# Performance work log

Hardware: AMD Instinct MI355X
Metric: run time of the kernel (lower is better)

## Reference

```python
import jax, jax.numpy as jnp
import numpy as np

EMBED = 128   # embed_dim
HEADS = 8
POINTS = 4
H_SP, W_SP = 51, 102   # hardcoded spatial_shapes in __init__
BEV = 100              # bev_res
HRES = 50              # height_res


def _make_ref_points():
    """Exact numpy replica of the spherical grid built in __init__."""
    eps = 1e-6
    x = np.linspace(-71 / 2, 71 / 2, BEV)
    y = np.linspace(-71 / 2, 71 / 2, BEV)
    z = np.linspace(-50 / 2, 50 / 2, HRES)
    gx, gy, gz = np.meshgrid(x, y, z, indexing='ij')
    phi = np.sign(gy + eps) * np.arccos(gx / (np.sqrt(gx ** 2 + gy ** 2) + eps))
    theta = np.arccos(gz / (np.sqrt(gx ** 2 + gy ** 2 + gz ** 2) + eps))
    phi = 2 * np.pi - phi
    phi[phi > 2 * np.pi] -= 2 * np.pi
    col = phi / (2 * np.pi)   # grd_col_cross
    row = theta / np.pi       # grd_row_cross
    ref = np.stack([col, row], axis=-1)              # (BEV, BEV, HRES, 2)
    ref = ref.transpose(2, 0, 1, 3).reshape(HRES, BEV * BEV, 2)
    return jnp.asarray(ref, dtype=jnp.float32)


def setup_inputs() -> dict:
    key = jax.random.key(0)
    ks = jax.random.split(key, 12)
    d = EMBED
    s = 0.02
    return {
        'query': jax.random.normal(ks[0], (1, BEV * BEV, d), jnp.float32),
        'value': jax.random.normal(ks[1], (1, H_SP * W_SP, d), jnp.float32),
        'ref_points': _make_ref_points(),
        'W_off': jax.random.normal(ks[2], (d, HEADS * POINTS * 2), jnp.float32) * s,
        'b_off': jax.random.normal(ks[3], (HEADS * POINTS * 2,), jnp.float32) * s,
        'W_attn': jax.random.normal(ks[4], (d, HEADS * POINTS), jnp.float32) * s,
        'b_attn': jax.random.normal(ks[5], (HEADS * POINTS,), jnp.float32) * s,
        'W_val': jax.random.normal(ks[6], (d, d), jnp.float32) * s,
        'b_val': jax.random.normal(ks[7], (d,), jnp.float32) * s,
        'W_out': jax.random.normal(ks[8], (d, d), jnp.float32) * s,
        'b_out': jax.random.normal(ks[9], (d,), jnp.float32) * s,
        'W_proj': jax.random.normal(ks[10], (d, 1), jnp.float32) * s,
        'b_proj': jax.random.normal(ks[11], (1,), jnp.float32) * s,
    }


def _bilinear_sample(vflat, loc):
    """grid_sample(bilinear, zero padding, align_corners=False).
    vflat: (B, H*W, hd) value maps; loc: (B, N, 2) normalized [0,1] (x,y)."""
    px = loc[..., 0] * W_SP - 0.5
    py = loc[..., 1] * H_SP - 0.5
    x0 = jnp.floor(px)
    y0 = jnp.floor(py)
    dx = (px - x0)[..., None]
    dy = (py - y0)[..., None]
    x0i = x0.astype(jnp.int32)
    y0i = y0.astype(jnp.int32)

    def gather(xi, yi):
        valid = (xi >= 0) & (xi < W_SP) & (yi >= 0) & (yi < H_SP)
        idx = jnp.clip(yi, 0, H_SP - 1) * W_SP + jnp.clip(xi, 0, W_SP - 1)
        v = jnp.take_along_axis(vflat, idx[..., None], axis=1)  # (B, N, hd)
        return v * valid[..., None].astype(vflat.dtype)

    v00 = gather(x0i, y0i)
    v01 = gather(x0i + 1, y0i)
    v10 = gather(x0i, y0i + 1)
    v11 = gather(x0i + 1, y0i + 1)
    return (v00 * (1 - dx) * (1 - dy) + v01 * dx * (1 - dy)
            + v10 * (1 - dx) * dy + v11 * dx * dy)


def reference(query, value, ref_points, W_off, b_off, W_attn, b_attn,
              W_val, b_val, W_out, b_out, W_proj, b_proj):
    bs, nq, d = query.shape
    hd = d // HEADS
    L = ref_points.shape[0]

    # query-dependent MSDA projections (identical across height levels)
    offsets = (query @ W_off + b_off).reshape(bs, nq, HEADS, POINTS, 2)
    aw = jax.nn.softmax((query @ W_attn + b_attn).reshape(bs, nq, HEADS, POINTS), axis=-1)
    awt = aw.transpose(0, 2, 1, 3)                              # (bs, heads, nq, points)
    v = (value @ W_val + b_val).reshape(bs, -1, HEADS, hd)
    vflat = v.transpose(0, 2, 1, 3).reshape(bs * HEADS, H_SP * W_SP, hd)
    norm = jnp.asarray([W_SP, H_SP], dtype=query.dtype)         # offset_normalizer [W, H]

    def per_level(ref):  # ref: (nq, 2) -> MSDA output with its internal residual
        loc = ref[None, :, None, None, :] + offsets / norm      # (bs, nq, heads, pts, 2)
        loc = loc.transpose(0, 2, 1, 3, 4).reshape(bs * HEADS, nq * POINTS, 2)
        samp = _bilinear_sample(vflat, loc).reshape(bs, HEADS, nq, POINTS, hd)
        out = jnp.einsum('bhnp,bhnpd->bnhd', awt, samp).reshape(bs, nq, d)
        return out @ W_out + b_out + query                      # mmcv MSDA adds identity

    grd = jax.vmap(per_level)(ref_points)                       # (L, bs, nq, d)
    grd_3d = grd.transpose(1, 2, 0, 3).reshape(bs, BEV, BEV, L, d)
    weights = jax.nn.softmax(grd_3d @ W_proj + b_proj, axis=3)  # (bs, BEV, BEV, L, 1)
    max_height_index = jnp.argmax(weights, axis=3)              # (bs, BEV, BEV, 1)
    grd_bev = (weights * grd_3d).sum(axis=3)                    # (bs, BEV, BEV, d)
    return grd_bev.reshape(bs, nq, d) + query, max_height_index
```

## Files before the change

### kernel.cpp

```cpp
#include <hip/hip_runtime.h>
#include <hip/hip_fp16.h>
#include <math.h>

#define EMBED   128
#define NHEADS  8
#define NPOINTS 4
#define HD      16
#define HSP     51
#define WSP     102
#define NPIX    (HSP * WSP)
#define NQ      10000
#define NLVL    50

struct h4v { __half2 a; __half2 b; };

__device__ __forceinline__ float4 h4_to_f4(h4v v) {
    const float2 lo = __half22float2(v.a);
    const float2 hi = __half22float2(v.b);
    float4 r; r.x = lo.x; r.y = lo.y; r.z = hi.x; r.w = hi.y;
    return r;
}

#define GRID_A ((NPIX + 7) / 8)
#define GRID_B (NQ / 8)

__global__ __launch_bounds__(256) void k_prep(
    const float* __restrict__ value,
    const float* __restrict__ Wv,
    const float* __restrict__ bv,
    const float* __restrict__ query,
    const float* __restrict__ Woff,
    const float* __restrict__ boff,
    const float* __restrict__ Wattn,
    const float* __restrict__ battn,
    const float* __restrict__ Wout,
    const float* __restrict__ Wproj,
    __half* __restrict__ vout,
    float* __restrict__ gout,
    float* __restrict__ off_out,
    float* __restrict__ aw_out) {
    const int b = blockIdx.x;
    const int t = threadIdx.x;
    __shared__ float srow[8][EMBED];
    __shared__ float4 u_s[32];

    if (b < GRID_A) {
        const int p   = t >> 5;
        const int s   = t & 31;
        const int pix = b * 8 + p;
        const int pl  = min(pix, NPIX - 1);
        *(float4*)&srow[p][s * 4] =
            *(const float4*)(value + (size_t)pl * EMBED + s * 4);
        if (t < 32) {
            float4 u4 = {0.f, 0.f, 0.f, 0.f};
            const float* w0 = Wout + (size_t)(t * 4 + 0) * EMBED;
            const float* w1 = Wout + (size_t)(t * 4 + 1) * EMBED;
            const float* w2 = Wout + (size_t)(t * 4 + 2) * EMBED;
            const float* w3 = Wout + (size_t)(t * 4 + 3) * EMBED;
#pragma unroll 4
            for (int d = 0; d < EMBED; d += 4) {
                const float4 wp = *(const float4*)(Wproj + d);
                const float4 a = *(const float4*)(w0 + d);
                const float4 c = *(const float4*)(w1 + d);
                const float4 e = *(const float4*)(w2 + d);
                const float4 f = *(const float4*)(w3 + d);
                u4.x = fmaf(a.x, wp.x, u4.x); u4.x = fmaf(a.y, wp.y, u4.x);
                u4.x = fmaf(a.z, wp.z, u4.x); u4.x = fmaf(a.w, wp.w, u4.x);
                u4.y = fmaf(c.x, wp.x, u4.y); u4.y = fmaf(c.y, wp.y, u4.y);
                u4.y = fmaf(c.z, wp.z, u4.y); u4.y = fmaf(c.w, wp.w, u4.y);
                u4.z = fmaf(e.x, wp.x, u4.z); u4.z = fmaf(e.y, wp.y, u4.z);
                u4.z = fmaf(e.z, wp.z, u4.z); u4.z = fmaf(e.w, wp.w, u4.z);
                u4.w = fmaf(f.x, wp.x, u4.w); u4.w = fmaf(f.y, wp.y, u4.w);
                u4.w = fmaf(f.z, wp.z, u4.w); u4.w = fmaf(f.w, wp.w, u4.w);
            }
            u_s[t] = u4;
        }
        __syncthreads();
        float4 acc = *(const float4*)(bv + s * 4);
        const float* vr = srow[p];
        const float* wp = Wv + s * 4;
#pragma unroll 8
        for (int k = 0; k < EMBED; ++k) {
            const float qv = vr[k];
            const float4 w4 = *(const float4*)(wp + (size_t)k * EMBED);
            acc.x = fmaf(qv, w4.x, acc.x);
            acc.y = fmaf(qv, w4.y, acc.y);
            acc.z = fmaf(qv, w4.z, acc.z);
            acc.w = fmaf(qv, w4.w, acc.w);
        }
        const float4 u4 = u_s[s];
        float gp = acc.x * u4.x;
        gp = fmaf(acc.y, u4.y, gp);
        gp = fmaf(acc.z, u4.z, gp);
        gp = fmaf(acc.w, u4.w, gp);
        gp += __shfl_xor(gp, 1, 64);
        gp += __shfl_xor(gp, 2, 64);
        if (pix < NPIX) {
            h4v hv;
            hv.a = __floats2half2_rn(acc.x, acc.y);
            hv.b = __floats2half2_rn(acc.z, acc.w);
            *(h4v*)(vout + (size_t)pix * EMBED + s * 4) = hv;
            if ((s & 3) == 0)
                gout[(size_t)pix * NHEADS + (s >> 2)] = gp;
        }
    } else if (b < GRID_A + GRID_B) {
        const int qi = t >> 5;
        const int s  = t & 31;
        const int q  = (b - GRID_A) * 8 + qi;
        *(float4*)&srow[qi][s * 4] =
            *(const float4*)(query + (size_t)q * EMBED + s * 4);
        __syncthreads();
        if (s < 24) {
            const float* vr = srow[qi];
            const float* wp;
            int wstride;
            float4 acc;
            if (s < 16) {
                wp = Woff + s * 4; wstride = 64;
                acc = *(const float4*)(boff + s * 4);
            } else {
                wp = Wattn + (s - 16) * 4; wstride = 32;
                acc = *(const float4*)(battn + (s - 16) * 4);
            }
#pragma unroll 8
            for (int k = 0; k < EMBED; ++k) {
                const float qv = vr[k];
                const float4 w4 = *(const float4*)(wp + (size_t)k * wstride);
                acc.x = fmaf(qv, w4.x, acc.x);
                acc.y = fmaf(qv, w4.y, acc.y);
                acc.z = fmaf(qv, w4.z, acc.z);
                acc.w = fmaf(qv, w4.w, acc.w);
            }
            if (s < 16) {
                *(float4*)(off_out + (size_t)q * 64 + s * 4) = acc;
            } else {
                const float mx = fmaxf(fmaxf(acc.x, acc.y), fmaxf(acc.z, acc.w));
                const float e0 = __expf(acc.x - mx), e1 = __expf(acc.y - mx);
                const float e2 = __expf(acc.z - mx), e3 = __expf(acc.w - mx);
                const float inv = 1.f / (e0 + e1 + e2 + e3);
                float4 r;
                r.x = e0 * inv; r.y = e1 * inv; r.z = e2 * inv; r.w = e3 * inv;
                *(float4*)(aw_out + (size_t)q * 32 + (s - 16) * 4) = r;
            }
        }
    }
}

__global__ __launch_bounds__(256, 4) void k_main(
    const float* __restrict__ query,
    const float* __restrict__ refp,
    const float* __restrict__ voff,
    const float* __restrict__ vaw,
    const __half* __restrict__ vflat,
    const float* __restrict__ gmap,
    const float* __restrict__ Wout,
    const float* __restrict__ bout,
    float* __restrict__ out0,
    float* __restrict__ out1) {
    const int t = threadIdx.x;
    const int qslot = t >> 7;
    const int w2 = (t >> 6) & 1;
    const int half = (t >> 5) & 1;
    const int sub = t & 31;
    const int h  = sub >> 2;
    const int c4 = sub & 3;
    const int q = blockIdx.x * 2 + qslot;

    __shared__ float  s_rpy[2][NLVL];
    __shared__ float4 s_acc[2][32];
    __shared__ float  s_z[2], s_m[2];
    __shared__ int    s_b[2];

    if (t < 2 * NLVL) {
        const int ql = t / NLVL, l = t - ql * NLVL;
        const int qq = blockIdx.x * 2 + ql;
        s_rpy[ql][l] = refp[((size_t)l * NQ + qq) * 2 + 1];
    }

    const float4* offp = (const float4*)(voff + (size_t)q * 64 + h * 8);
    const float4 o01 = offp[0];
    const float4 o23 = offp[1];
    const float4 awv4 = *(const float4*)(vaw + (size_t)q * 32 + h * 4);
    const float rpx = refp[(size_t)q * 2];
    const h4v* vbase = (const h4v*)vflat + sub;

    const float offx[4] = {o01.x, o01.z, o23.x, o23.z};
    const float offy[4] = {o01.y, o01.w, o23.y, o23.w};
    const float awv[4]  = {awv4.x, awv4.y, awv4.z, awv4.w};

    float wx0[NPOINTS], wx1[NPOINTS], oyc[NPOINTS];
    int xo0[NPOINTS], xo1[NPOINTS];
#pragma unroll
    for (int p = 0; p < NPOINTS; ++p) {
        const float px = fmaf(rpx, (float)WSP, offx[p]) - 0.5f;
        const float fx = floorf(px);
        const float dx = px - fx;
        const int x0 = (int)fx, x1 = x0 + 1;
        const float a = awv[p];
        wx0[p] = ((unsigned)x0 < (unsigned)WSP) ? a * (1.f - dx) : 0.f;
        wx1[p] = ((unsigned)x1 < (unsigned)WSP) ? a * dx : 0.f;
        xo0[p] = min(max(x0, 0), WSP - 1) * 32;
        xo1[p] = min(max(x1, 0), WSP - 1) * 32;
        oyc[p] = offy[p] - 0.5f;
    }

    const float offx_c = (c4 == 0) ? o01.x : (c4 == 1) ? o01.z : (c4 == 2) ? o23.x : o23.z;
    const float offy_c = (c4 == 0) ? o01.y : (c4 == 1) ? o01.w : (c4 == 2) ? o23.y : o23.w;
    const float a_c    = (c4 == 0) ? awv4.x : (c4 == 1) ? awv4.y : (c4 == 2) ? awv4.z : awv4.w;
    const float pxc = fmaf(rpx, (float)WSP, offx_c) - 0.5f;
    const float fxc = floorf(pxc);
    const float dxc = pxc - fxc;
    const int x0c = (int)fxc, x1c = x0c + 1;
    const float gwx0 = ((unsigned)x0c < (unsigned)WSP) ? a_c * (1.f - dxc) : 0.f;
    const float gwx1 = ((unsigned)x1c < (unsigned)WSP) ? a_c * dxc : 0.f;
    const int gx0 = min(max(x0c, 0), WSP - 1) * NHEADS + h;
    const int gx1 = min(max(x1c, 0), WSP - 1) * NHEADS + h;
    const float oyc_c = offy_c - 0.5f;

    __syncthreads();

    float4 acc = {0.f, 0.f, 0.f, 0.f};
    float Z = 0.f, m = -1e30f;
    int best = 0;

#pragma unroll 1
    for (int i = 0; i < 13; ++i) {
        if (4 * i + (w2 << 1) >= NLVL) break;
        const int l = 4 * i + (w2 << 1) + half;
        const float rpy = s_rpy[qslot][l];

        const float pyc = fmaf(rpy, (float)HSP, oyc_c);
        const float fyc = floorf(pyc);
        const float dyc = pyc - fyc;
        const int gy0 = (int)fyc, gy1 = gy0 + 1;
        const float gt0 = ((unsigned)gy0 < (unsigned)HSP) ? (1.f - dyc) : 0.f;
        const float gt1 = ((unsigned)gy1 < (unsigned)HSP) ? dyc : 0.f;
        const int gr0 = min(max(gy0, 0), HSP - 1) * (WSP * NHEADS);
        const int gr1 = min(max(gy1, 0), HSP - 1) * (WSP * NHEADS);
        const float g00 = gmap[gr0 + gx0];
        const float g01 = gmap[gr0 + gx1];
        const float g10 = gmap[gr1 + gx0];
        const float g11 = gmap[gr1 + gx1];

        h4v v00[NPOINTS], v01[NPOINTS], v10[NPOINTS], v11[NPOINTS];
        float w00[NPOINTS], w01[NPOINTS], w10[NPOINTS], w11[NPOINTS];
#pragma unroll
        for (int p = 0; p < NPOINTS; ++p) {
            const float py = fmaf(rpy, (float)HSP, oyc[p]);
            const float fy = floorf(py);
            const float dy = py - fy;
            const int y0 = (int)fy, y1 = y0 + 1;
            const float t0 = ((unsigned)y0 < (unsigned)HSP) ? (1.f - dy) : 0.f;
            const float t1 = ((unsigned)y1 < (unsigned)HSP) ? dy : 0.f;
            const int rb0 = min(max(y0, 0), HSP - 1) * (WSP * 32);
            const int rb1 = min(max(y1, 0), HSP - 1) * (WSP * 32);
            v00[p] = vbase[rb0 + xo0[p]];
            v01[p] = vbase[rb0 + xo1[p]];
            v10[p] = vbase[rb1 + xo0[p]];
            v11[p] = vbase[rb1 + xo1[p]];
            w00[p] = wx0[p] * t0;
            w01[p] = wx1[p] * t0;
            w10[p] = wx0[p] * t1;
            w11[p] = wx1[p] * t1;
        }
        float4 s = {0.f, 0.f, 0.f, 0.f};
#pragma unroll
        for (int p = 0; p < NPOINTS; ++p) {
            const float4 f00 = h4_to_f4(v00[p]);
            const float4 f01 = h4_to_f4(v01[p]);
            const float4 f10 = h4_to_f4(v10[p]);
            const float4 f11 = h4_to_f4(v11[p]);
            s.x = fmaf(w00[p], f00.x, s.x); s.y = fmaf(w00[p], f00.y, s.y);
            s.z = fmaf(w00[p], f00.z, s.z); s.w = fmaf(w00[p], f00.w, s.w);
            s.x = fmaf(w01[p], f01.x, s.x); s.y = fmaf(w01[p], f01.y, s.y);
            s.z = fmaf(w01[p], f01.z, s.z); s.w = fmaf(w01[p], f01.w, s.w);
            s.x = fmaf(w10[p], f10.x, s.x); s.y = fmaf(w10[p], f10.y, s.y);
            s.z = fmaf(w10[p], f10.z, s.z); s.w = fmaf(w10[p], f10.w, s.w);
            s.x = fmaf(w11[p], f11.x, s.x); s.y = fmaf(w11[p], f11.y, s.y);
            s.z = fmaf(w11[p], f11.z, s.z); s.w = fmaf(w11[p], f11.w, s.w);
        }
        float row0 = gwx0 * g00; row0 = fmaf(gwx1, g01, row0);
        float row1 = gwx0 * g10; row1 = fmaf(gwx1, g11, row1);
        float part = gt0 * row0; part = fmaf(gt1, row1, part);
#pragma unroll
        for (int d = 1; d < 32; d <<= 1)
            part += __shfl_xor(part, d, 64);
        const float e = __expf(part);
        Z += e;
        acc.x = fmaf(e, s.x, acc.x);
        acc.y = fmaf(e, s.y, acc.y);
        acc.z = fmaf(e, s.z, acc.z);
        acc.w = fmaf(e, s.w, acc.w);
        best = (part > m) ? l : best;
        m = fmaxf(part, m);
    }

    {
        const float mo = __shfl_xor(m, 32, 64);
        const int   bo = __shfl_xor(best, 32, 64);
        const float Zo = __shfl_xor(Z, 32, 64);
        const float ax = __shfl_xor(acc.x, 32, 64);
        const float ay = __shfl_xor(acc.y, 32, 64);
        const float az = __shfl_xor(acc.z, 32, 64);
        const float aw_ = __shfl_xor(acc.w, 32, 64);
        const bool takeOther = (mo > m) || (mo == m && bo < best);
        best = takeOther ? bo : best;
        m = fmaxf(m, mo);
        Z += Zo;
        acc.x += ax; acc.y += ay; acc.z += az; acc.w += aw_;
    }

    if (w2 == 1) {
        if (half == 0) s_acc[qslot][sub] = acc;
        if ((t & 63) == 0) { s_z[qslot] = Z; s_m[qslot] = m; s_b[qslot] = best; }
    }
    __syncthreads();

    if (w2 == 0) {
        const float4 ao = s_acc[qslot][sub];
        const float Zo = s_z[qslot];
        const float mo = s_m[qslot];
        const int   bo = s_b[qslot];
        const bool takeOther = (mo > m) || (mo == m && bo < best);
        best = takeOther ? bo : best;
        Z += Zo;
        acc.x += ao.x; acc.y += ao.y; acc.z += ao.z; acc.w += ao.w;

        const float inv = 1.f / Z;
        if (half == 0) {
            float4 sv;
            sv.x = acc.x * inv; sv.y = acc.y * inv;
            sv.z = acc.z * inv; sv.w = acc.w * inv;
            s_acc[qslot][sub] = sv;
            if (sub == 0) out1[q] = (float)best;
        }

        const int dpb = sub * 4;
        float4 r = {0.f, 0.f, 0.f, 0.f};
        if (half == 0) {
            const float4 b4 = *(const float4*)(bout + dpb);
            const float4 q4 = *(const float4*)(query + (size_t)q * EMBED + dpb);
            r.x = fmaf(2.f, q4.x, b4.x);
            r.y = fmaf(2.f, q4.y, b4.y);
            r.z = fmaf(2.f, q4.z, b4.z);
            r.w = fmaf(2.f, q4.w, b4.w);
        }
        const float4* srow = s_acc[qslot];
        const int cg0 = half * 16;
#pragma unroll 4
        for (int cg = cg0; cg < cg0 + 16; ++cg) {
            const float4 s4 = srow[cg];
            const float4 w0 = *(const float4*)(Wout + (size_t)(cg * 4 + 0) * EMBED + dpb);
            const float4 w1 = *(const float4*)(Wout + (size_t)(cg * 4 + 1) * EMBED + dpb);
            const float4 w2v = *(const float4*)(Wout + (size_t)(cg * 4 + 2) * EMBED + dpb);
            const float4 w3 = *(const float4*)(Wout + (size_t)(cg * 4 + 3) * EMBED + dpb);
            r.x = fmaf(s4.x, w0.x, r.x); r.y = fmaf(s4.x, w0.y, r.y);
            r.z = fmaf(s4.x, w0.z, r.z); r.w = fmaf(s4.x, w0.w, r.w);
            r.x = fmaf(s4.y, w1.x, r.x); r.y = fmaf(s4.y, w1.y, r.y);
            r.z = fmaf(s4.y, w1.z, r.z); r.w = fmaf(s4.y, w1.w, r.w);
            r.x = fmaf(s4.z, w2v.x, r.x); r.y = fmaf(s4.z, w2v.y, r.y);
            r.z = fmaf(s4.z, w2v.z, r.z); r.w = fmaf(s4.z, w2v.w, r.w);
            r.x = fmaf(s4.w, w3.x, r.x); r.y = fmaf(s4.w, w3.y, r.y);
            r.z = fmaf(s4.w, w3.z, r.z); r.w = fmaf(s4.w, w3.w, r.w);
        }
        {
            const float rx = __shfl_xor(r.x, 32, 64);
            const float ry = __shfl_xor(r.y, 32, 64);
            const float rz = __shfl_xor(r.z, 32, 64);
            const float rw = __shfl_xor(r.w, 32, 64);
            r.x += rx; r.y += ry; r.z += rz; r.w += rw;
        }
        if (half == 0)
            *(float4*)(out0 + (size_t)q * EMBED + dpb) = r;
    }
}

extern "C" void kernel_launch(void* const* d_in, const int* in_sizes, int n_in,
                              void* d_out, int out_size, void* d_ws, size_t ws_size,
                              hipStream_t stream) {
    const float* query = (const float*)d_in[0];
    const float* value = (const float*)d_in[1];
    const float* refp  = (const float*)d_in[2];
    const float* Woff  = (const float*)d_in[3];
    const float* boff  = (const float*)d_in[4];
    const float* Wattn = (const float*)d_in[5];
    const float* battn = (const float*)d_in[6];
    const float* Wval  = (const float*)d_in[7];
    const float* bval  = (const float*)d_in[8];
    const float* Wout  = (const float*)d_in[9];
    const float* bout  = (const float*)d_in[10];
    const float* Wproj = (const float*)d_in[11];

    float* ws = (float*)d_ws;
    __half* ws_v = (__half*)ws;
    float* ws_g   = ws + (size_t)NPIX * EMBED / 2;
    float* ws_off = ws_g + (size_t)NPIX * NHEADS;
    float* ws_aw  = ws_off + (size_t)NQ * 64;

    float* out0 = (float*)d_out;
    float* out1 = out0 + (size_t)NQ * EMBED;

    hipLaunchKernelGGL(k_prep, dim3(GRID_A + GRID_B), dim3(256), 0, stream,
                       value, Wval, bval, query, Woff, boff, Wattn, battn,
                       Wout, Wproj, ws_v, ws_g, ws_off, ws_aw);
    hipLaunchKernelGGL(k_main, dim3(NQ / 2), dim3(256), 0, stream,
                       query, refp, ws_off, ws_aw, ws_v, ws_g, Wout, bout,
                       out0, out1);
}
```

Measured before the change: 286.3 us.

## Zero-pad value and gate maps to drop bilinear bounds checks

The projected value map and the per-head gate map are written into a padded grid (54x105) whose border slots hold zeros. Sample coordinates are then clamped with a med3 into [-1, W] and [-1, H], so every corner read lands in the padded buffer. This removes the per-corner validity tests, clamps and weight masking from the hot sampling loop. It costs a slightly larger prep workload and workspace, and relies on the zero border reproducing zero-padding semantics.

```diff
diff --git a/kernel.cpp b/kernel.cpp
--- a/kernel.cpp
+++ b/kernel.cpp
@@ -12,16 +12,15 @@
 #define NQ      10000
 #define NLVL    50
 
+#define PROW 54
+#define PCOL 105
+#define NSLOT (PROW * PCOL)
+#define ROWH  (PCOL * 32)
+#define GROW  (PCOL * NHEADS)
+
 struct h4v { __half2 a; __half2 b; };
 
-__device__ __forceinline__ float4 h4_to_f4(h4v v) {
-    const float2 lo = __half22float2(v.a);
-    const float2 hi = __half22float2(v.b);
-    float4 r; r.x = lo.x; r.y = lo.y; r.z = hi.x; r.w = hi.y;
-    return r;
-}
-
-#define GRID_A ((NPIX + 7) / 8)
+#define GRID_A ((NSLOT + 7) / 8)
 #define GRID_B (NQ / 8)
 
 __global__ __launch_bounds__(256) void k_prep(
@@ -45,12 +44,18 @@
     __shared__ float4 u_s[32];
 
     if (b < GRID_A) {
-        const int p   = t >> 5;
-        const int s   = t & 31;
-        const int pix = b * 8 + p;
-        const int pl  = min(pix, NPIX - 1);
-        *(float4*)&srow[p][s * 4] =
-            *(const float4*)(value + (size_t)pl * EMBED + s * 4);
+        const int p    = t >> 5;
+        const int s    = t & 31;
+        const int slot = b * 8 + p;
+        const int prow = slot / PCOL;
+        const int pcol = slot - prow * PCOL;
+        const bool inb   = slot < NSLOT;
+        const bool valid = inb && prow >= 1 && prow <= HSP
+                               && pcol >= 1 && pcol <= WSP;
+        const int pix = (prow - 1) * WSP + (pcol - 1);
+        if (valid)
+            *(float4*)&srow[p][s * 4] =
+                *(const float4*)(value + (size_t)pix * EMBED + s * 4);
         if (t < 32) {
             float4 u4 = {0.f, 0.f, 0.f, 0.f};
             const float* w0 = Wout + (size_t)(t * 4 + 0) * EMBED;
@@ -76,17 +81,20 @@
             u_s[t] = u4;
         }
         __syncthreads();
-        float4 acc = *(const float4*)(bv + s * 4);
-        const float* vr = srow[p];
-        const float* wp = Wv + s * 4;
+        float4 acc = {0.f, 0.f, 0.f, 0.f};
+        if (valid) {
+            acc = *(const float4*)(bv + s * 4);
+            const float* vr = srow[p];
+            const float* wp = Wv + s * 4;
 #pragma unroll 8
-        for (int k = 0; k < EMBED; ++k) {
-            const float qv = vr[k];
-            const float4 w4 = *(const float4*)(wp + (size_t)k * EMBED);
-            acc.x = fmaf(qv, w4.x, acc.x);
-            acc.y = fmaf(qv, w4.y, acc.y);
-            acc.z = fmaf(qv, w4.z, acc.z);
-            acc.w = fmaf(qv, w4.w, acc.w);
+            for (int k = 0; k < EMBED; ++k) {
+                const float qv = vr[k];
+                const float4 w4 = *(const float4*)(wp + (size_t)k * EMBED);
+                acc.x = fmaf(qv, w4.x, acc.x);
+                acc.y = fmaf(qv, w4.y, acc.y);
+                acc.z = fmaf(qv, w4.z, acc.z);
+                acc.w = fmaf(qv, w4.w, acc.w);
+            }
         }
         const float4 u4 = u_s[s];
         float gp = acc.x * u4.x;
@@ -95,13 +103,13 @@
         gp = fmaf(acc.w, u4.w, gp);
         gp += __shfl_xor(gp, 1, 64);
         gp += __shfl_xor(gp, 2, 64);
-        if (pix < NPIX) {
+        if (inb) {
             h4v hv;
             hv.a = __floats2half2_rn(acc.x, acc.y);
             hv.b = __floats2half2_rn(acc.z, acc.w);
-            *(h4v*)(vout + (size_t)pix * EMBED + s * 4) = hv;
+            *(h4v*)(vout + (size_t)slot * EMBED + s * 4) = hv;
             if ((s & 3) == 0)
-                gout[(size_t)pix * NHEADS + (s >> 2)] = gp;
+                gout[(size_t)slot * NHEADS + (s >> 2)] = gp;
         }
     } else if (b < GRID_A + GRID_B) {
         const int qi = t >> 5;
@@ -182,39 +190,38 @@
     const float4 o23 = offp[1];
     const float4 awv4 = *(const float4*)(vaw + (size_t)q * 32 + h * 4);
     const float rpx = refp[(size_t)q * 2];
-    const h4v* vbase = (const h4v*)vflat + sub;
+    const h4v* vflat_h4 = (const h4v*)vflat;
 
     const float offx[4] = {o01.x, o01.z, o23.x, o23.z};
     const float offy[4] = {o01.y, o01.w, o23.y, o23.w};
     const float awv[4]  = {awv4.x, awv4.y, awv4.z, awv4.w};
 
     float wx0[NPOINTS], wx1[NPOINTS], oyc[NPOINTS];
-    int xo0[NPOINTS], xo1[NPOINTS];
+    int xa[NPOINTS];
 #pragma unroll
     for (int p = 0; p < NPOINTS; ++p) {
         const float px = fmaf(rpx, (float)WSP, offx[p]) - 0.5f;
-        const float fx = floorf(px);
-        const float dx = px - fx;
-        const int x0 = (int)fx, x1 = x0 + 1;
+        const float pxc = __builtin_amdgcn_fmed3f(px, -1.f, (float)WSP);
+        const float fx = floorf(pxc);
+        const float dx = pxc - fx;
+        const int x0 = (int)fx;
         const float a = awv[p];
-        wx0[p] = ((unsigned)x0 < (unsigned)WSP) ? a * (1.f - dx) : 0.f;
-        wx1[p] = ((unsigned)x1 < (unsigned)WSP) ? a * dx : 0.f;
-        xo0[p] = min(max(x0, 0), WSP - 1) * 32;
-        xo1[p] = min(max(x1, 0), WSP - 1) * 32;
+        wx0[p] = a * (1.f - dx);
+        wx1[p] = a * dx;
+        xa[p] = (x0 + 1) * 32 + ROWH + sub;
         oyc[p] = offy[p] - 0.5f;
     }
 
     const float offx_c = (c4 == 0) ? o01.x : (c4 == 1) ? o01.z : (c4 == 2) ? o23.x : o23.z;
     const float offy_c = (c4 == 0) ? o01.y : (c4 == 1) ? o01.w : (c4 == 2) ? o23.y : o23.w;
     const float a_c    = (c4 == 0) ? awv4.x : (c4 == 1) ? awv4.y : (c4 == 2) ? awv4.z : awv4.w;
-    const float pxc = fmaf(rpx, (float)WSP, offx_c) - 0.5f;
+    const float pxc = __builtin_amdgcn_fmed3f(
+        fmaf(rpx, (float)WSP, offx_c) - 0.5f, -1.f, (float)WSP);
     const float fxc = floorf(pxc);
     const float dxc = pxc - fxc;
-    const int x0c = (int)fxc, x1c = x0c + 1;
-    const float gwx0 = ((unsigned)x0c < (unsigned)WSP) ? a_c * (1.f - dxc) : 0.f;
-    const float gwx1 = ((unsigned)x1c < (unsigned)WSP) ? a_c * dxc : 0.f;
-    const int gx0 = min(max(x0c, 0), WSP - 1) * NHEADS + h;
-    const int gx1 = min(max(x1c, 0), WSP - 1) * NHEADS + h;
+    const float gwx0 = a_c * (1.f - dxc);
+    const float gwx1 = a_c * dxc;
+    const int gxa = ((int)fxc + 1) * NHEADS + h + GROW;
     const float oyc_c = offy_c - 0.5f;
 
     __syncthreads();
@@ -229,59 +236,60 @@
         const int l = 4 * i + (w2 << 1) + half;
         const float rpy = s_rpy[qslot][l];
 
-        const float pyc = fmaf(rpy, (float)HSP, oyc_c);
+        const float pyc = __builtin_amdgcn_fmed3f(
+            fmaf(rpy, (float)HSP, oyc_c), -1.f, (float)HSP);
         const float fyc = floorf(pyc);
         const float dyc = pyc - fyc;
-        const int gy0 = (int)fyc, gy1 = gy0 + 1;
-        const float gt0 = ((unsigned)gy0 < (unsigned)HSP) ? (1.f - dyc) : 0.f;
-        const float gt1 = ((unsigned)gy1 < (unsigned)HSP) ? dyc : 0.f;
-        const int gr0 = min(max(gy0, 0), HSP - 1) * (WSP * NHEADS);
-        const int gr1 = min(max(gy1, 0), HSP - 1) * (WSP * NHEADS);
-        const float g00 = gmap[gr0 + gx0];
-        const float g01 = gmap[gr0 + gx1];
-        const float g10 = gmap[gr1 + gx0];
-        const float g11 = gmap[gr1 + gx1];
+        const int gi0 = (int)fyc * GROW + gxa;
+        const float g00 = gmap[gi0];
+        const float g01 = gmap[gi0 + NHEADS];
+        const float g10 = gmap[gi0 + GROW];
+        const float g11 = gmap[gi0 + GROW + NHEADS];
 
         h4v v00[NPOINTS], v01[NPOINTS], v10[NPOINTS], v11[NPOINTS];
         float w00[NPOINTS], w01[NPOINTS], w10[NPOINTS], w11[NPOINTS];
 #pragma unroll
         for (int p = 0; p < NPOINTS; ++p) {
             const float py = fmaf(rpy, (float)HSP, oyc[p]);
-            const float fy = floorf(py);
-            const float dy = py - fy;
-            const int y0 = (int)fy, y1 = y0 + 1;
-            const float t0 = ((unsigned)y0 < (unsigned)HSP) ? (1.f - dy) : 0.f;
-            const float t1 = ((unsigned)y1 < (unsigned)HSP) ? dy : 0.f;
-            const int rb0 = min(max(y0, 0), HSP - 1) * (WSP * 32);
-            const int rb1 = min(max(y1, 0), HSP - 1) * (WSP * 32);
-            v00[p] = vbase[rb0 + xo0[p]];
-            v01[p] = vbase[rb0 + xo1[p]];
-            v10[p] = vbase[rb1 + xo0[p]];
-            v11[p] = vbase[rb1 + xo1[p]];
+            const float pyc2 = __builtin_amdgcn_fmed3f(py, -1.f, (float)HSP);
+            const float fy = floorf(pyc2);
+            const float dy = pyc2 - fy;
+            const int y0 = (int)fy;
+            const int i0 = y0 * ROWH + xa[p];
+            const int i1 = i0 + ROWH;
+            const float t0 = 1.f - dy;
+            v00[p] = vflat_h4[i0];
+            v01[p] = vflat_h4[i0 + 32];
+            v10[p] = vflat_h4[i1];
+            v11[p] = vflat_h4[i1 + 32];
             w00[p] = wx0[p] * t0;
             w01[p] = wx1[p] * t0;
-            w10[p] = wx0[p] * t1;
-            w11[p] = wx1[p] * t1;
+            w10[p] = wx0[p] * dy;
+            w11[p] = wx1[p] * dy;
         }
         float4 s = {0.f, 0.f, 0.f, 0.f};
 #pragma unroll
         for (int p = 0; p < NPOINTS; ++p) {
-            const float4 f00 = h4_to_f4(v00[p]);
-            const float4 f01 = h4_to_f4(v01[p]);
-            const float4 f10 = h4_to_f4(v10[p]);
-            const float4 f11 = h4_to_f4(v11[p]);
-            s.x = fmaf(w00[p], f00.x, s.x); s.y = fmaf(w00[p], f00.y, s.y);
-            s.z = fmaf(w00[p], f00.z, s.z); s.w = fmaf(w00[p], f00.w, s.w);
-            s.x = fmaf(w01[p], f01.x, s.x); s.y = fmaf(w01[p], f01.y, s.y);
-            s.z = fmaf(w01[p], f01.z, s.z); s.w = fmaf(w01[p], f01.w, s.w);
-            s.x = fmaf(w10[p], f10.x, s.x); s.y = fmaf(w10[p], f10.y, s.y);
-            s.z = fmaf(w10[p], f10.z, s.z); s.w = fmaf(w10[p], f10.w, s.w);
-            s.x = fmaf(w11[p], f11.x, s.x); s.y = fmaf(w11[p], f11.y, s.y);
-            s.z = fmaf(w11[p], f11.z, s.z); s.w = fmaf(w11[p], f11.w, s.w);
+            s.x = fmaf(w00[p], __half2float(__low2half(v00[p].a)), s.x);
+            s.y = fmaf(w00[p], __half2float(__high2half(v00[p].a)), s.y);
+            s.z = fmaf(w00[p], __half2float(__low2half(v00[p].b)), s.z);
+            s.w = fmaf(w00[p], __half2float(__high2half(v00[p].b)), s.w);
+            s.x = fmaf(w01[p], __half2float(__low2half(v01[p].a)), s.x);
+            s.y = fmaf(w01[p], __half2float(__high2half(v01[p].a)), s.y);
+            s.z = fmaf(w01[p], __half2float(__low2half(v01[p].b)), s.z);
+            s.w = fmaf(w01[p], __half2float(__high2half(v01[p].b)), s.w);
+            s.x = fmaf(w10[p], __half2float(__low2half(v10[p].a)), s.x);
+            s.y = fmaf(w10[p], __half2float(__high2half(v10[p].a)), s.y);
+            s.z = fmaf(w10[p], __half2float(__low2half(v10[p].b)), s.z);
+            s.w = fmaf(w10[p], __half2float(__high2half(v10[p].b)), s.w);
+            s.x = fmaf(w11[p], __half2float(__low2half(v11[p].a)), s.x);
+            s.y = fmaf(w11[p], __half2float(__high2half(v11[p].a)), s.y);
+            s.z = fmaf(w11[p], __half2float(__low2half(v11[p].b)), s.z);
+            s.w = fmaf(w11[p], __half2float(__high2half(v11[p].b)), s.w);
         }
         float row0 = gwx0 * g00; row0 = fmaf(gwx1, g01, row0);
         float row1 = gwx0 * g10; row1 = fmaf(gwx1, g11, row1);
-        float part = gt0 * row0; part = fmaf(gt1, row1, part);
+        float part = (1.f - dyc) * row0; part = fmaf(dyc, row1, part);
 #pragma unroll
         for (int d = 1; d < 32; d <<= 1)
             part += __shfl_xor(part, d, 64);
@@ -393,8 +401,8 @@
 
     float* ws = (float*)d_ws;
     __half* ws_v = (__half*)ws;
-    float* ws_g   = ws + (size_t)NPIX * EMBED / 2;
-    float* ws_off = ws_g + (size_t)NPIX * NHEADS;
+    float* ws_g   = ws + (size_t)NSLOT * EMBED / 2;
+    float* ws_off = ws_g + (size_t)NSLOT * NHEADS;
     float* ws_aw  = ws_off + (size_t)NQ * 64;
 
     float* out0 = (float*)d_out;
```

Measured after the change: 286.8 us. About the same (+0.2%).
